# Optimization experiments

Measured on AMD Instinct MI355X. Metric: run time of the kernel, lower is better.

Reference implementation:

```python
import jax, jax.numpy as jnp
import numpy as np

B, C, H, W = 64, 32, 112, 112
RANK = 3


def setup_inputs() -> dict:
    key = jax.random.key(0)
    k1, k2, k3, k4, k5 = jax.random.split(key, 5)
    N = H * W  # 12544
    return {
        "x": jax.random.uniform(k1, (B, C, H, W), dtype=jnp.float32),
        "p_buffer": jax.random.normal(k2, (B, N, RANK), dtype=jnp.float32),
        "q_buffer": jax.random.normal(k3, (B, C, RANK), dtype=jnp.float32),
        "grad_p_buffer": jax.random.normal(k4, (B, N, RANK), dtype=jnp.float32),
        "grad_q_buffer": jax.random.normal(k5, (B, C, RANK), dtype=jnp.float32),
        "n_iter": 2,
    }


def _power_svd(X, P, Q, n_iter):
    # X: [b, c, n]; P: [b, n, r]; Q: [b, c, r]
    for i in range(n_iter):
        if i == n_iter - 1:
            P = jnp.linalg.qr(P)[0]  # batched reduced QR, tall-skinny (n x r)
        Q = jnp.einsum('bcn,bnr->bcr', X, P)
        if i == n_iter - 1:
            Q = jnp.linalg.qr(Q)[0]  # batched reduced QR (c x r)
        P = jnp.einsum('bcn,bcr->bnr', X, Q)  # X^T @ Q
    return P, Q


def reference(x, p_buffer, q_buffer, grad_p_buffer, grad_q_buffer, n_iter):
    shape = x.shape
    X = x.reshape(shape[0], shape[1], -1)  # [B, C, H*W]
    P, Q = _power_svd(X, p_buffer, q_buffer, n_iter)
    # low-rank reconstruction Q @ P^T, back to original shape
    return jnp.einsum('bcr,bnr->bcn', Q, P).reshape(shape)
```

## Files before the change

### kernel.cpp

```cpp
#include <hip/hip_runtime.h>
#include <math.h>

#define N_HW 12544
#define TN 128
#define NCH 98
#define KB 24

#define WS_P1 0
#define WS_P2 (64 * KB * 1024)
#define WS_QP (2 * 64 * KB * 1024)
#define WS_U  (WS_QP + 64 * KB * 96)

typedef __attribute__((ext_vector_type(8)))  short short8;
typedef __attribute__((ext_vector_type(16))) float f32x16;
typedef __attribute__((ext_vector_type(4)))  float f32x4;

#define MFMA(a, b, c) __builtin_amdgcn_mfma_f32_32x32x16_bf16((a), (b), (c), 0, 0, 0)

__device__ __forceinline__ void split3(float f, ushort& h, ushort& m, ushort& l) {
    unsigned u = __builtin_bit_cast(unsigned, f);
    h = (ushort)(u >> 16);
    float fh = __builtin_bit_cast(float, u & 0xffff0000u);
    float rm = f - fh;
    unsigned um = __builtin_bit_cast(unsigned, rm);
    m = (ushort)(um >> 16);
    float fm = __builtin_bit_cast(float, um & 0xffff0000u);
    float rl = rm - fm;
    l = (ushort)(__builtin_bit_cast(unsigned, rl) >> 16);
}

__device__ __forceinline__ int xq(int c, int o) {
    return c * 16 + ((o & 8) | ((o ^ c) & 7));
}

__global__ __launch_bounds__(256)
void k1_gram(const float* __restrict__ x, const float* __restrict__ p,
             float* __restrict__ P1, float* __restrict__ P2, float* __restrict__ Qp)
{
    const int b = blockIdx.y, kb = blockIdx.x;
    const int tid = threadIdx.x;
    const int lane = tid & 63, wave = tid >> 6;

    __shared__ uint4 XS[3 * 512];
    __shared__ alignas(16) ushort PTH[3 * TN], PTM[3 * TN], PTL[3 * TN];
    float* dmp = (float*)XS;

    const int c = tid >> 3, oc = tid & 7;
    const float* xrow = x + ((size_t)b * 32 + c) * N_HW;
    const float* pbat = p + (size_t)b * N_HW * 3;

    f32x16 D1 = {0,0,0,0,0,0,0,0,0,0,0,0,0,0,0,0};
    f32x16 D2 = {0,0,0,0,0,0,0,0,0,0,0,0,0,0,0,0};
    f32x16 DQ = {0,0,0,0,0,0,0,0,0,0,0,0,0,0,0,0};
    const int cl = lane & 31, g = lane >> 5;
    const int rr = (cl < 3) ? cl : 0;

    float4 pre[4];
    float prep[3];
    int j = kb;
    {
        const float4* xr = (const float4*)(xrow + (size_t)j * TN);
        pre[0] = xr[2 * oc];      pre[1] = xr[2 * oc + 1];
        pre[2] = xr[2 * oc + 16]; pre[3] = xr[2 * oc + 17];
        if (tid < TN) {
            const float* pb = pbat + (size_t)(j * TN + tid) * 3;
            prep[0] = pb[0]; prep[1] = pb[1]; prep[2] = pb[2];
        }
    }

    while (true) {
        #pragma unroll
        for (int t = 0; t < 2; ++t) {
            const int o = oc + 8 * t;
            float4 f0 = pre[2 * t], f1 = pre[2 * t + 1];
            float fv[8] = {f0.x, f0.y, f0.z, f0.w, f1.x, f1.y, f1.z, f1.w};
            unsigned hw[4], mw[4], lw[4];
            #pragma unroll
            for (int i = 0; i < 4; ++i) {
                ushort h0, m0, l0, h1, m1, l1;
                split3(fv[2 * i],     h0, m0, l0);
                split3(fv[2 * i + 1], h1, m1, l1);
                hw[i] = (unsigned)h0 | ((unsigned)h1 << 16);
                mw[i] = (unsigned)m0 | ((unsigned)m1 << 16);
                lw[i] = (unsigned)l0 | ((unsigned)l1 << 16);
            }
            const int s = xq(c, o);
            XS[s]        = make_uint4(hw[0], hw[1], hw[2], hw[3]);
            XS[512 + s]  = make_uint4(mw[0], mw[1], mw[2], mw[3]);
            XS[1024 + s] = make_uint4(lw[0], lw[1], lw[2], lw[3]);
        }
        if (tid < TN) {
            #pragma unroll
            for (int r = 0; r < 3; ++r) {
                ushort h, m, l;
                split3(prep[r], h, m, l);
                PTH[r * TN + tid] = h; PTM[r * TN + tid] = m; PTL[r * TN + tid] = l;
            }
        }

        const int jn = j + KB;
        const bool more = (jn < NCH);
        if (more) {
            const float4* xr = (const float4*)(xrow + (size_t)jn * TN);
            pre[0] = xr[2 * oc];      pre[1] = xr[2 * oc + 1];
            pre[2] = xr[2 * oc + 16]; pre[3] = xr[2 * oc + 17];
            if (tid < TN) {
                const float* pb = pbat + (size_t)(jn * TN + tid) * 3;
                prep[0] = pb[0]; prep[1] = pb[1]; prep[2] = pb[2];
            }
        }
        __syncthreads();

        for (int s = wave; s < 8; s += 4) {
            const int sl = xq(cl, 2 * s + g);
            short8 xh = __builtin_bit_cast(short8, XS[sl]);
            short8 xm = __builtin_bit_cast(short8, XS[512 + sl]);
            short8 xl = __builtin_bit_cast(short8, XS[1024 + sl]);
            const int po = rr * TN + 16 * s + 8 * g;
            short8 ph = *(const short8*)&PTH[po];
            short8 pm = *(const short8*)&PTM[po];
            short8 pl = *(const short8*)&PTL[po];
            D1 = MFMA(xh, xh, D1);
            D1 = MFMA(xm, xm, D1);
            D2 = MFMA(xh, xm, D2);
            D2 = MFMA(xh, xl, D2);
            DQ = MFMA(xh, ph, DQ);
            DQ = MFMA(xh, pm, DQ);
            DQ = MFMA(xm, ph, DQ);
            DQ = MFMA(xh, pl, DQ);
            DQ = MFMA(xl, ph, DQ);
            DQ = MFMA(xm, pm, DQ);
        }

        if (!more) break;
        j = jn;
        __syncthreads();
    }

    #define DUMP_REDUCE_G(D, gdst)                                                         \
        __syncthreads();                                                                   \
        _Pragma("unroll")                                                                  \
        for (int i = 0; i < 4; ++i)                                                        \
            *(float4*)&dmp[tid * 20 + 4 * i] =                                             \
                make_float4((D)[4*i], (D)[4*i+1], (D)[4*i+2], (D)[4*i+3]);                 \
        __syncthreads();                                                                   \
        _Pragma("unroll")                                                                  \
        for (int it = 0; it < 4; ++it) {                                                   \
            const int e = tid + 256 * it;                                                  \
            const int r = e >> 5, co = e & 31;                                             \
            const int ln = co + 32 * ((r >> 2) & 1);                                       \
            const int rg = (r & 3) + 4 * (r >> 3);                                         \
            (gdst)[e] = dmp[ln * 20 + rg] + dmp[(64 + ln) * 20 + rg]                       \
                      + dmp[(128 + ln) * 20 + rg] + dmp[(192 + ln) * 20 + rg];             \
        }

    float* p1 = P1 + ((size_t)b * KB + kb) * 1024;
    float* p2 = P2 + ((size_t)b * KB + kb) * 1024;
    DUMP_REDUCE_G(D1, p1)
    DUMP_REDUCE_G(D2, p2)

    __syncthreads();
    #pragma unroll
    for (int i = 0; i < 4; ++i)
        *(float4*)&dmp[tid * 20 + 4 * i] = make_float4(DQ[4*i], DQ[4*i+1], DQ[4*i+2], DQ[4*i+3]);
    __syncthreads();
    if (tid < 96) {
        const int c2 = tid / 3, r2 = tid - 3 * c2;
        const int ln = r2 + 32 * ((c2 >> 2) & 1);
        const int rg = (c2 & 3) + 4 * (c2 >> 3);
        float s = dmp[ln * 20 + rg] + dmp[(64 + ln) * 20 + rg]
                + dmp[(128 + ln) * 20 + rg] + dmp[(192 + ln) * 20 + rg];
        Qp[((size_t)b * KB + kb) * 96 + tid] = s;
    }
}

__global__ __launch_bounds__(256)
void k2_solve(const float* __restrict__ P1, const float* __restrict__ P2,
              const float* __restrict__ Qp, float* __restrict__ Uo)
{
    const int b = blockIdx.x, tid = threadIdx.x;
    __shared__ float S[1024], A2[1024];
    __shared__ float Qv[96], V[96], G[6], L[6];

    float a1[4] = {0.f, 0.f, 0.f, 0.f}, a2[4] = {0.f, 0.f, 0.f, 0.f};
    const float* p1 = P1 + (size_t)b * KB * 1024;
    const float* p2 = P2 + (size_t)b * KB * 1024;
    for (int kb = 0; kb < KB; ++kb) {
        #pragma unroll
        for (int i = 0; i < 4; ++i) {
            a1[i] += p1[kb * 1024 + tid + 256 * i];
            a2[i] += p2[kb * 1024 + tid + 256 * i];
        }
    }
    #pragma unroll
    for (int i = 0; i < 4; ++i) A2[tid + 256 * i] = a2[i];
    if (tid < 96) {
        const float* qp = Qp + (size_t)b * KB * 96;
        float q = 0.f;
        for (int kb = 0; kb < KB; ++kb) q += qp[kb * 96 + tid];
        Qv[tid] = q;
    }
    __syncthreads();
    #pragma unroll
    for (int i = 0; i < 4; ++i) {
        const int e = tid + 256 * i;
        const int et = ((e & 31) << 5) | (e >> 5);
        S[e] = a1[i] + a2[i] + A2[et];
    }
    __syncthreads();

    if (tid < 96) {
        const int c = tid / 3, r = tid % 3;
        float s = 0.f;
        #pragma unroll 8
        for (int cc = 0; cc < 32; ++cc) s += S[c * 32 + cc] * Qv[cc * 3 + r];
        V[tid] = s;
    }
    for (int round = 0; round < 2; ++round) {
        __syncthreads();
        if (tid < 6) {
            const int r = (tid > 2) ? 2 : ((tid > 0) ? 1 : 0);
            const int s = tid - (r * (r + 1)) / 2;
            float g = 0.f;
            for (int c = 0; c < 32; ++c) g += V[c * 3 + r] * V[c * 3 + s];
            G[tid] = g;
        }
        __syncthreads();
        if (tid == 0) {
            const float l00 = sqrtf(G[0]);
            const float l10 = G[1] / l00, l20 = G[3] / l00;
            const float l11 = sqrtf(G[2] - l10 * l10);
            const float l21 = (G[4] - l20 * l10) / l11;
            const float l22 = sqrtf(G[5] - l20 * l20 - l21 * l21);
            L[0] = l00; L[1] = l10; L[2] = l11; L[3] = l20; L[4] = l21; L[5] = l22;
        }
        __syncthreads();
        if (tid < 32) {
            const float v0 = V[tid * 3 + 0], v1 = V[tid * 3 + 1], v2 = V[tid * 3 + 2];
            const float u0 = v0 / L[0];
            const float u1 = (v1 - L[1] * u0) / L[2];
            const float u2 = (v2 - L[3] * u0 - L[4] * u1) / L[5];
            V[tid * 3 + 0] = u0; V[tid * 3 + 1] = u1; V[tid * 3 + 2] = u2;
        }
    }
    __syncthreads();
    if (tid < 32) {
        Uo[(size_t)b * 128 + tid * 4 + 0] = V[tid * 3 + 0];
        Uo[(size_t)b * 128 + tid * 4 + 1] = V[tid * 3 + 1];
        Uo[(size_t)b * 128 + tid * 4 + 2] = V[tid * 3 + 2];
        Uo[(size_t)b * 128 + tid * 4 + 3] = 0.f;
    }
}

__global__ __launch_bounds__(256)
void k3_out(const float* __restrict__ x, const float* __restrict__ Uw,
            float* __restrict__ out)
{
    const int b = blockIdx.y, tid = threadIdx.x;
    __shared__ float Us[32][4];
    if (tid < 128) ((float*)Us)[tid] = Uw[(size_t)b * 128 + tid];
    __syncthreads();
    const int g = blockIdx.x * 256 + tid;
    if (g >= N_HW / 4) return;

    const float* Xb = x   + (size_t)b * 32 * N_HW + 4 * (size_t)g;
    float*       Ob = out + (size_t)b * 32 * N_HW + 4 * (size_t)g;

    float t0x = 0, t0y = 0, t0z = 0, t0w = 0;
    float t1x = 0, t1y = 0, t1z = 0, t1w = 0;
    float t2x = 0, t2y = 0, t2z = 0, t2w = 0;
    #pragma unroll 16
    for (int c = 0; c < 32; ++c) {
        float4 xv = *(const float4*)(Xb + (size_t)c * N_HW);
        const float u0 = Us[c][0], u1 = Us[c][1], u2 = Us[c][2];
        t0x += u0 * xv.x; t0y += u0 * xv.y; t0z += u0 * xv.z; t0w += u0 * xv.w;
        t1x += u1 * xv.x; t1y += u1 * xv.y; t1z += u1 * xv.z; t1w += u1 * xv.w;
        t2x += u2 * xv.x; t2y += u2 * xv.y; t2z += u2 * xv.z; t2w += u2 * xv.w;
    }
    #pragma unroll 16
    for (int c = 0; c < 32; ++c) {
        const float u0 = Us[c][0], u1 = Us[c][1], u2 = Us[c][2];
        f32x4 o;
        o.x = u0 * t0x + u1 * t1x + u2 * t2x;
        o.y = u0 * t0y + u1 * t1y + u2 * t2y;
        o.z = u0 * t0z + u1 * t1z + u2 * t2z;
        o.w = u0 * t0w + u1 * t1w + u2 * t2w;
        __builtin_nontemporal_store(o, (f32x4*)(Ob + (size_t)c * N_HW));
    }
}

extern "C" void kernel_launch(void* const* d_in, const int* in_sizes, int n_in,
                              void* d_out, int out_size, void* d_ws, size_t ws_size,
                              hipStream_t stream)
{
    const float* x = (const float*)d_in[0];
    const float* p = (const float*)d_in[1];
    float* ws = (float*)d_ws;
    float* P1 = ws + WS_P1;
    float* P2 = ws + WS_P2;
    float* Qp = ws + WS_QP;
    float* U  = ws + WS_U;
    float* out = (float*)d_out;

    hipLaunchKernelGGL(k1_gram, dim3(KB, 64), dim3(256), 0, stream, x, p, P1, P2, Qp);
    hipLaunchKernelGGL(k2_solve, dim3(64), dim3(256), 0, stream, P1, P2, Qp, U);
    hipLaunchKernelGGL(k3_out, dim3((N_HW / 4 + 255) / 256, 64), dim3(256), 0, stream, x, U, out);
}
```

Measured before the change: 231.8 us.

## Double-buffer register prefetch in k1 and vectorize partial-sum loads in k2

The k1 chunk loop now keeps two register sets (XA/XB) and prefetches two chunks ahead, alternating stage and MFMA phases. It also replaces __syncthreads with a raw lgkmcnt wait plus s_barrier and raises wave priority around the MFMA block. In k2, the partial-sum reduction now reads float4 vectors with a partly unrolled loop instead of strided scalar loads. The deeper prefetch adds register pressure and could lower occupancy, and the hand-written barrier depends on the LDS wait being sufficient for correctness.

```diff
diff --git a/kernel.cpp b/kernel.cpp
--- a/kernel.cpp
+++ b/kernel.cpp
@@ -16,6 +16,13 @@
 typedef __attribute__((ext_vector_type(4)))  float f32x4;
 
 #define MFMA(a, b, c) __builtin_amdgcn_mfma_f32_32x32x16_bf16((a), (b), (c), 0, 0, 0)
+
+#define LDS_BAR()                                                \
+    do {                                                         \
+        asm volatile("s_waitcnt lgkmcnt(0)" ::: "memory");       \
+        __builtin_amdgcn_s_barrier();                            \
+        asm volatile("" ::: "memory");                           \
+    } while (0)
 
 __device__ __forceinline__ void split3(float f, ushort& h, ushort& m, ushort& l) {
     unsigned u = __builtin_bit_cast(unsigned, f);
@@ -55,86 +62,105 @@
     const int cl = lane & 31, g = lane >> 5;
     const int rr = (cl < 3) ? cl : 0;
 
-    float4 pre[4];
-    float prep[3];
-    int j = kb;
-    {
-        const float4* xr = (const float4*)(xrow + (size_t)j * TN);
-        pre[0] = xr[2 * oc];      pre[1] = xr[2 * oc + 1];
-        pre[2] = xr[2 * oc + 16]; pre[3] = xr[2 * oc + 17];
-        if (tid < TN) {
-            const float* pb = pbat + (size_t)(j * TN + tid) * 3;
-            prep[0] = pb[0]; prep[1] = pb[1]; prep[2] = pb[2];
-        }
-    }
+#define LOADX(PX, jj)                                                          \
+    do {                                                                       \
+        const float4* xr = (const float4*)(xrow + (size_t)(jj) * TN);          \
+        PX[0] = xr[2 * oc];      PX[1] = xr[2 * oc + 1];                       \
+        PX[2] = xr[2 * oc + 16]; PX[3] = xr[2 * oc + 17];                      \
+    } while (0)
+
+#define LOADP(PP, jj)                                                          \
+    do { if (tid < TN) {                                                       \
+        const float* pb = pbat + (size_t)((jj) * TN + tid) * 3;                \
+        PP[0] = pb[0]; PP[1] = pb[1]; PP[2] = pb[2];                           \
+    } } while (0)
+
+#define STAGE(PX, PP)                                                          \
+    do {                                                                       \
+        _Pragma("unroll")                                                      \
+        for (int t = 0; t < 2; ++t) {                                          \
+            const int o = oc + 8 * t;                                          \
+            float4 f0 = PX[2 * t], f1 = PX[2 * t + 1];                         \
+            float fv[8] = {f0.x, f0.y, f0.z, f0.w, f1.x, f1.y, f1.z, f1.w};    \
+            unsigned hw[4], mw[4], lw[4];                                      \
+            _Pragma("unroll")                                                  \
+            for (int i = 0; i < 4; ++i) {                                      \
+                ushort h0, m0, l0, h1, m1, l1;                                 \
+                split3(fv[2 * i],     h0, m0, l0);                             \
+                split3(fv[2 * i + 1], h1, m1, l1);                             \
+                hw[i] = (unsigned)h0 | ((unsigned)h1 << 16);                   \
+                mw[i] = (unsigned)m0 | ((unsigned)m1 << 16);                   \
+                lw[i] = (unsigned)l0 | ((unsigned)l1 << 16);                   \
+            }                                                                  \
+            const int s = xq(c, o);                                            \
+            XS[s]        = make_uint4(hw[0], hw[1], hw[2], hw[3]);             \
+            XS[512 + s]  = make_uint4(mw[0], mw[1], mw[2], mw[3]);             \
+            XS[1024 + s] = make_uint4(lw[0], lw[1], lw[2], lw[3]);             \
+        }                                                                      \
+        if (tid < TN) {                                                        \
+            _Pragma("unroll")                                                  \
+            for (int r = 0; r < 3; ++r) {                                      \
+                ushort h, m, l;                                                \
+                split3(PP[r], h, m, l);                                        \
+                PTH[r * TN + tid] = h; PTM[r * TN + tid] = m;                  \
+                PTL[r * TN + tid] = l;                                         \
+            }                                                                  \
+        }                                                                      \
+    } while (0)
+
+#define MFMA_PHASE()                                                           \
+    do {                                                                       \
+        __builtin_amdgcn_s_setprio(1);                                         \
+        for (int s = wave; s < 8; s += 4) {                                    \
+            const int sl = xq(cl, 2 * s + g);                                  \
+            short8 xh = __builtin_bit_cast(short8, XS[sl]);                    \
+            short8 xm = __builtin_bit_cast(short8, XS[512 + sl]);              \
+            short8 xl = __builtin_bit_cast(short8, XS[1024 + sl]);             \
+            const int po = rr * TN + 16 * s + 8 * g;                           \
+            short8 ph = *(const short8*)&PTH[po];                              \
+            short8 pm = *(const short8*)&PTM[po];                              \
+            short8 pl = *(const short8*)&PTL[po];                              \
+            D1 = MFMA(xh, xh, D1);                                             \
+            D1 = MFMA(xm, xm, D1);                                             \
+            D2 = MFMA(xh, xm, D2);                                             \
+            D2 = MFMA(xh, xl, D2);                                             \
+            DQ = MFMA(xh, ph, DQ);                                             \
+            DQ = MFMA(xh, pm, DQ);                                             \
+            DQ = MFMA(xm, ph, DQ);                                             \
+            DQ = MFMA(xh, pl, DQ);                                             \
+            DQ = MFMA(xl, ph, DQ);                                             \
+            DQ = MFMA(xm, pm, DQ);                                             \
+        }                                                                      \
+        __builtin_amdgcn_s_setprio(0);                                         \
+    } while (0)
+
+    float4 XA[4], XB[4];
+    float  PA[3], PB[3];
+    int j = kb, jB = kb + KB;
+    LOADX(XA, j); LOADP(PA, j);
+    bool hasB = (jB < NCH);
+    if (hasB) { LOADX(XB, jB); LOADP(PB, jB); }
 
     while (true) {
-        #pragma unroll
-        for (int t = 0; t < 2; ++t) {
-            const int o = oc + 8 * t;
-            float4 f0 = pre[2 * t], f1 = pre[2 * t + 1];
-            float fv[8] = {f0.x, f0.y, f0.z, f0.w, f1.x, f1.y, f1.z, f1.w};
-            unsigned hw[4], mw[4], lw[4];
-            #pragma unroll
-            for (int i = 0; i < 4; ++i) {
-                ushort h0, m0, l0, h1, m1, l1;
-                split3(fv[2 * i],     h0, m0, l0);
-                split3(fv[2 * i + 1], h1, m1, l1);
-                hw[i] = (unsigned)h0 | ((unsigned)h1 << 16);
-                mw[i] = (unsigned)m0 | ((unsigned)m1 << 16);
-                lw[i] = (unsigned)l0 | ((unsigned)l1 << 16);
-            }
-            const int s = xq(c, o);
-            XS[s]        = make_uint4(hw[0], hw[1], hw[2], hw[3]);
-            XS[512 + s]  = make_uint4(mw[0], mw[1], mw[2], mw[3]);
-            XS[1024 + s] = make_uint4(lw[0], lw[1], lw[2], lw[3]);
-        }
-        if (tid < TN) {
-            #pragma unroll
-            for (int r = 0; r < 3; ++r) {
-                ushort h, m, l;
-                split3(prep[r], h, m, l);
-                PTH[r * TN + tid] = h; PTM[r * TN + tid] = m; PTL[r * TN + tid] = l;
-            }
-        }
-
-        const int jn = j + KB;
-        const bool more = (jn < NCH);
-        if (more) {
-            const float4* xr = (const float4*)(xrow + (size_t)jn * TN);
-            pre[0] = xr[2 * oc];      pre[1] = xr[2 * oc + 1];
-            pre[2] = xr[2 * oc + 16]; pre[3] = xr[2 * oc + 17];
-            if (tid < TN) {
-                const float* pb = pbat + (size_t)(jn * TN + tid) * 3;
-                prep[0] = pb[0]; prep[1] = pb[1]; prep[2] = pb[2];
-            }
-        }
-        __syncthreads();
-
-        for (int s = wave; s < 8; s += 4) {
-            const int sl = xq(cl, 2 * s + g);
-            short8 xh = __builtin_bit_cast(short8, XS[sl]);
-            short8 xm = __builtin_bit_cast(short8, XS[512 + sl]);
-            short8 xl = __builtin_bit_cast(short8, XS[1024 + sl]);
-            const int po = rr * TN + 16 * s + 8 * g;
-            short8 ph = *(const short8*)&PTH[po];
-            short8 pm = *(const short8*)&PTM[po];
-            short8 pl = *(const short8*)&PTL[po];
-            D1 = MFMA(xh, xh, D1);
-            D1 = MFMA(xm, xm, D1);
-            D2 = MFMA(xh, xm, D2);
-            D2 = MFMA(xh, xl, D2);
-            DQ = MFMA(xh, ph, DQ);
-            DQ = MFMA(xh, pm, DQ);
-            DQ = MFMA(xm, ph, DQ);
-            DQ = MFMA(xh, pl, DQ);
-            DQ = MFMA(xl, ph, DQ);
-            DQ = MFMA(xm, pm, DQ);
-        }
-
-        if (!more) break;
-        j = jn;
-        __syncthreads();
+        STAGE(XA, PA);
+        const int jn = j + 2 * KB;
+        const bool preA = (jn < NCH);
+        if (preA) { LOADX(XA, jn); LOADP(PA, jn); }
+        LDS_BAR();
+        MFMA_PHASE();
+        if (!hasB) break;
+        LDS_BAR();
+
+        STAGE(XB, PB);
+        const int jn2 = jB + 2 * KB;
+        const bool preB = (jn2 < NCH);
+        if (preB) { LOADX(XB, jn2); LOADP(PB, jn2); }
+        LDS_BAR();
+        MFMA_PHASE();
+        if (!preA) break;
+        LDS_BAR();
+
+        j = jn; jB = jn2; hasB = preB;
     }
 
     #define DUMP_REDUCE_G(D, gdst)                                                         \
@@ -182,30 +208,33 @@
     __shared__ float S[1024], A2[1024];
     __shared__ float Qv[96], V[96], G[6], L[6];
 
-    float a1[4] = {0.f, 0.f, 0.f, 0.f}, a2[4] = {0.f, 0.f, 0.f, 0.f};
-    const float* p1 = P1 + (size_t)b * KB * 1024;
-    const float* p2 = P2 + (size_t)b * KB * 1024;
+    f32x4 a1 = {0.f, 0.f, 0.f, 0.f}, a2 = {0.f, 0.f, 0.f, 0.f};
+    const float4* p1 = (const float4*)(P1 + (size_t)b * KB * 1024);
+    const float4* p2 = (const float4*)(P2 + (size_t)b * KB * 1024);
+    #pragma unroll 4
     for (int kb = 0; kb < KB; ++kb) {
-        #pragma unroll
-        for (int i = 0; i < 4; ++i) {
-            a1[i] += p1[kb * 1024 + tid + 256 * i];
-            a2[i] += p2[kb * 1024 + tid + 256 * i];
-        }
-    }
-    #pragma unroll
-    for (int i = 0; i < 4; ++i) A2[tid + 256 * i] = a2[i];
+        float4 v1 = p1[kb * 256 + tid];
+        float4 v2 = p2[kb * 256 + tid];
+        a1.x += v1.x; a1.y += v1.y; a1.z += v1.z; a1.w += v1.w;
+        a2.x += v2.x; a2.y += v2.y; a2.z += v2.z; a2.w += v2.w;
+    }
+    A2[4 * tid + 0] = a2.x; A2[4 * tid + 1] = a2.y;
+    A2[4 * tid + 2] = a2.z; A2[4 * tid + 3] = a2.w;
     if (tid < 96) {
         const float* qp = Qp + (size_t)b * KB * 96;
         float q = 0.f;
+        #pragma unroll 4
         for (int kb = 0; kb < KB; ++kb) q += qp[kb * 96 + tid];
         Qv[tid] = q;
     }
     __syncthreads();
     #pragma unroll
     for (int i = 0; i < 4; ++i) {
-        const int e = tid + 256 * i;
+        const int e = 4 * tid + i;
         const int et = ((e & 31) << 5) | (e >> 5);
-        S[e] = a1[i] + a2[i] + A2[et];
+        S[e] = ((i == 0) ? a1.x : (i == 1) ? a1.y : (i == 2) ? a1.z : a1.w)
+             + ((i == 0) ? a2.x : (i == 1) ? a2.y : (i == 2) ? a2.z : a2.w)
+             + A2[et];
     }
     __syncthreads();
 
```

Result: no change. 231.6 us (-0.1%).
